# Optimization experiments

Hardware: AMD Instinct MI355X
Metric: run time of the kernel (lower is better)

The kernel has to match this reference:

```python
import jax, jax.numpy as jnp
import numpy as np

B, T, V, E, H, NL = 32, 64, 32000, 300, 512, 2
NF, D = 128, 32  # num midi frames, midi_frame_dim
LSTM_IN = E + D  # 332


def setup_inputs() -> dict:
    key = jax.random.key(0)
    ks = jax.random.split(key, 20)
    s = 0.05
    inp = {
        "input_seq": jax.random.randint(ks[0], (B, T), 0, V),
        "midi_sequence": jax.random.normal(ks[1], (B, NF, D), jnp.float32),
        "emb": jax.random.normal(ks[2], (V, E), jnp.float32) * s,
        "mp_w": jax.random.normal(ks[3], (D, D), jnp.float32) * s,
        "mp_b": jnp.zeros((D,), jnp.float32),
        "wh": jax.random.normal(ks[4], (H, H), jnp.float32) * s,
        "wm": jax.random.normal(ks[5], (H, D), jnp.float32) * s,
        "v": jax.random.normal(ks[6], (1, H), jnp.float32) * s,
        "w_ih0": jax.random.normal(ks[7], (4 * H, LSTM_IN), jnp.float32) * s,
        "w_hh0": jax.random.normal(ks[8], (4 * H, H), jnp.float32) * s,
        "b_ih0": jnp.zeros((4 * H,), jnp.float32),
        "b_hh0": jnp.zeros((4 * H,), jnp.float32),
        "w_ih1": jax.random.normal(ks[9], (4 * H, H), jnp.float32) * s,
        "w_hh1": jax.random.normal(ks[10], (4 * H, H), jnp.float32) * s,
        "b_ih1": jnp.zeros((4 * H,), jnp.float32),
        "b_hh1": jnp.zeros((4 * H,), jnp.float32),
        "fc_w": jax.random.uniform(ks[11], (V, H), jnp.float32, -0.1, 0.1),
        "fc_b": jnp.zeros((V,), jnp.float32),
    }
    return inp


def _lstm_cell(x, hp, cp, wih, whh, bih, bhh):
    # PyTorch gate order: i, f, g, o
    g = x @ wih.T + hp @ whh.T + bih + bhh
    i, f, gg, o = jnp.split(g, 4, axis=-1)
    cn = jax.nn.sigmoid(f) * cp + jax.nn.sigmoid(i) * jnp.tanh(gg)
    hn = jax.nn.sigmoid(o) * jnp.tanh(cn)
    return hn, cn


def reference(input_seq, midi_sequence, emb, mp_w, mp_b, wh, wm, v,
              w_ih0, w_hh0, b_ih0, b_hh0, w_ih1, w_hh1, b_ih1, b_hh1,
              fc_w, fc_b):
    embeddings = emb[input_seq]  # [B,T,E] (dropout = identity in eval)
    midi_proj = jax.nn.relu(jnp.einsum('bfd,ed->bfe', midi_sequence, mp_w) + mp_b)  # [B,NF,D]
    midi_key = jnp.einsum('bfd,hd->bfh', midi_proj, wm)  # precomputed W_m(midi_proj)

    h0 = jnp.zeros((NL, B, H), embeddings.dtype)
    c0 = jnp.zeros((NL, B, H), embeddings.dtype)

    def step(carry, x_t):
        h, c = carry
        h_top = h[-1]  # [B,H]
        energy = jnp.tanh((h_top @ wh.T)[:, None, :] + midi_key)  # [B,NF,H]
        scores = jnp.einsum('bfh,h->bf', energy, v[0])
        attn = jax.nn.softmax(scores, axis=-1)  # [B,NF]
        ctx = jnp.einsum('bf,bfd->bd', attn, midi_proj)  # [B,D]
        x = jnp.concatenate([x_t, ctx], axis=-1)  # [B,E+D]
        h1, c1 = _lstm_cell(x, h[0], c[0], w_ih0, w_hh0, b_ih0, b_hh0)
        h2, c2 = _lstm_cell(h1, h[1], c[1], w_ih1, w_hh1, b_ih1, b_hh1)
        return (jnp.stack([h1, h2]), jnp.stack([c1, c2])), (h2, attn)

    (hF, cF), (outs, attns) = jax.lax.scan(step, (h0, c0), embeddings.transpose(1, 0, 2))
    lstm_out = outs.transpose(1, 0, 2)  # [B,T,H]
    logits = lstm_out @ fc_w.T + fc_b  # [B,T,V]
    return logits, (hF, cF), attns.transpose(1, 0, 2)
```

## Files before the change

### kernel.cpp

```cpp
#include <hip/hip_runtime.h>
#include <hip/hip_bf16.h>

#define Bsz 32
#define Tn  64
#define Vn  32000
#define En  300
#define Hn  512
#define NFn 128
#define Dn  32
#define G4  2048
#define LIN 332
#define NWG 256

#define OFF_MPROJ 0
#define OFF_E0    (OFF_MPROJ + 131072)
#define OFF_PG0B  (OFF_E0 + 4194304)
#define OFF_H1T   (OFF_PG0B + 65536)
#define OFF_H2T0  (OFF_H1T + 16384)
#define OFF_H2T1  (OFF_H2T0 + 16384)
#define OFF_H2BB  (OFF_H2T1 + 16384)
#define OFF_C1T   (OFF_H2BB + 16384)
#define OFF_C2T   (OFF_C1T + 16384)
#define OFF_FLG   (OFF_C2T + 16384)
#define OFF_DONE  (OFF_FLG + 4096)
#define OFF_VC    (OFF_DONE + 256)
#define OFF_MKEY  (OFF_VC + 16)
#define OFF_WHT   (OFF_MKEY + 2097152)
#define OFF_WCTX  (OFF_WHT + 262144)
#define OFF_X     (OFF_WCTX + 65536)
#define OFF_W0    (OFF_X + 655360)
#define OFF_HBF   OFF_X
#define OFF_FCWBF (OFF_X + 524288)

#define O_H1S  0
#define O_H2S  1048576
#define O_QS   2113536
#define O_CTXP 3162112
#define O_DENP 3686400
#define O_ES   3702784

#define OUT_HF  65536000
#define OUT_CF  65568768
#define OUT_ATT 65601536

#define L_HS2   0
#define L_HS1   4096
#define L_GL    8192
#define L_PG0   8480
#define L_C1    8736
#define L_C2    8800
#define L_CTX   8864
#define L_DEN   9128
#define L_QL    9136
#define L_VL    9664
#define L_SP    10192
#define L_ESL   10464
#define L_CP    10480
#define L_W0    11024
#define L_MK    27408
#define L_WH    35856
#define SCAN_LDS_FLOATS 39952
#define SCAN_LDS_BYTES  (SCAN_LDS_FLOATS*4)

typedef __attribute__((ext_vector_type(8))) short short8;
typedef __attribute__((ext_vector_type(4))) float f32x4;
typedef unsigned short u16;

__device__ __forceinline__ float frcp(float x){ return __builtin_amdgcn_rcpf(x); }
__device__ __forceinline__ float ftanh(float x){
  float e = __expf(2.0f*x);
  return 1.0f - 2.0f*frcp(e+1.0f);
}
__device__ __forceinline__ float fsig(float x){
  return frcp(1.0f + __expf(-x));
}
__device__ __forceinline__ u16 f2bf(float f){
  __hip_bfloat16 h = __float2bfloat16(f);
  u16 r; __builtin_memcpy(&r, &h, 2); return r;
}

__device__ __forceinline__ float ldc1(const float* p){
  return __hip_atomic_load(p, __ATOMIC_RELAXED, __HIP_MEMORY_SCOPE_AGENT);
}
__device__ __forceinline__ void stc1(float* p, float v){
  __hip_atomic_store(p, v, __ATOMIC_RELAXED, __HIP_MEMORY_SCOPE_AGENT);
}

__device__ __forceinline__ void flag_store(float* ws, int c, int slot, float v){
  stc1(ws + OFF_FLG + c*256 + slot*4, v);
}
__device__ __forceinline__ void aggregate(float* ws, int c, float tgt, int tid){
  if (tid < 64){
    const float* fl = ws + OFF_FLG + c*256;
    unsigned cc = 0;
    while (true){
      float v = ldc1(fl + tid*4);
      if (__ballot(v >= tgt) == ~0ull) break;
      if (++cc >= (1u<<22)) break;
    }
    if (tid == 0) stc1(ws + OFF_DONE + c*16, tgt);
  }
}
__device__ __forceinline__ void waitD(float* ws, int c, float tgt){
  __syncthreads();
  if (threadIdx.x == 0){
    unsigned cc = 0;
    while (ldc1(ws + OFF_DONE + c*16) < tgt){
      if (++cc >= (1u<<24)) break;
    }
  }
  __syncthreads();
  asm volatile("" ::: "memory");
}

__device__ __forceinline__ float redux32(float (&v)[32], int L){
  #pragma unroll
  for (int i=0;i<5;i++){
    const int m = 1<<i, h = 16>>i;
    const bool up = (L & m);
    #pragma unroll
    for (int u=0; u<h; u++){
      float send = up ? v[u] : v[u+h];
      float keep = up ? v[u+h] : v[u];
      v[u] = keep + __shfl_xor(send, m, 64);
    }
  }
  v[0] += __shfl_xor(v[0], 32, 64);
  return v[0];
}
__device__ __forceinline__ float redux16(float (&v)[16], int L){
  #pragma unroll
  for (int i=0;i<4;i++){
    const int m = 1<<i, h = 8>>i;
    const bool up = (L & m);
    #pragma unroll
    for (int u=0; u<h; u++){
      float send = up ? v[u] : v[u+h];
      float keep = up ? v[u+h] : v[u];
      v[u] = keep + __shfl_xor(send, m, 64);
    }
  }
  v[0] += __shfl_xor(v[0], 16, 64);
  v[0] += __shfl_xor(v[0], 32, 64);
  return v[0];
}

__global__ __launch_bounds__(1024) void p1_midi(
    const float* __restrict__ midi, const float* __restrict__ mp_w,
    const float* __restrict__ mp_b, const float* __restrict__ wm,
    float* __restrict__ ws)
{
  __shared__ float ms[NFn*Dn];
  __shared__ float pj[NFn*33];
  __shared__ float mpw[Dn*33];
  __shared__ float mpb[Dn];
  int b = blockIdx.x, tid = threadIdx.x;
  for (int i=tid;i<NFn*Dn;i+=1024) ms[i] = midi[b*NFn*Dn + i];
  { int e = tid>>5, d = tid&31; mpw[e*33+d] = mp_w[tid]; }
  if (tid < Dn) mpb[tid] = mp_b[tid];
  __syncthreads();
  float* mproj = ws + OFF_MPROJ;
  for (int i=tid;i<NFn*Dn;i+=1024){
    int f = i>>5, e = i&31;
    float a = mpb[e];
    #pragma unroll
    for (int d=0;d<Dn;d++) a += ms[f*32+d]*mpw[e*33+d];
    a = fmaxf(a, 0.0f);
    pj[f*33+e] = a;
    mproj[b*NFn*Dn + i] = a;
  }
  __syncthreads();
  int h = tid & 511, fh = tid >> 9;
  float wreg[32];
  #pragma unroll
  for (int d=0;d<32;d++) wreg[d] = wm[h*32+d];
  float* mkf = ws + OFF_MKEY + b*(NFn*Hn);
  for (int ff=0; ff<64; ff++){
    int f = fh*64 + ff;
    float a = 0.f;
    #pragma unroll
    for (int d=0;d<32;d++) a += pj[f*33+d]*wreg[d];
    mkf[f*512 + h] = a;
  }
}

__global__ __launch_bounds__(256) void p2a_x(
    const int* __restrict__ seq, const float* __restrict__ emb,
    float* __restrict__ ws)
{
  int idx = blockIdx.x*256 + threadIdx.x;
  int bt = idx / 80, c4 = idx - bt*80;
  int b = bt & 31, t = bt >> 5;
  float4 x = {0.f,0.f,0.f,0.f};
  if (c4 < 75){
    int s = seq[b*Tn + t];
    x = *(const float4*)(emb + (long)s*En + c4*4);
  }
  *(float4*)(ws + OFF_X + bt*320 + c4*4) = x;
}

__global__ __launch_bounds__(256) void p2b_w(
    const float* __restrict__ wih0, float* __restrict__ ws)
{
  int idx = blockIdx.x*256 + threadIdx.x;
  int j = idx / 80, c4 = idx - j*80;
  float4 x = {0.f,0.f,0.f,0.f};
  if (c4 < 75) x = *(const float4*)(wih0 + (long)j*LIN + c4*4);
  *(float4*)(ws + OFF_W0 + j*320 + c4*4) = x;
}

__global__ __launch_bounds__(256) void p2c_e0(
    const float* __restrict__ ws_c, const float* __restrict__ bih0,
    const float* __restrict__ bhh0, float* __restrict__ ws)
{
  const float* A  = ws_c + OFF_W0;
  const float* Bm = ws_c + OFF_X;
  __shared__ float Al[32][132];
  __shared__ float Bl[32][132];
  int tid = threadIdx.x;
  int j0t = blockIdx.x*128, bt0 = blockIdx.y*128;
  int tx = tid & 15, ty = tid >> 4;
  float acc[8][8];
  #pragma unroll
  for (int i=0;i<8;i++)
    #pragma unroll
    for (int j=0;j<8;j++) acc[i][j] = 0.f;

  int m = tid >> 1;
  int kq = (tid & 1) * 16;
  for (int kk=0; kk<320; kk+=32){
    __syncthreads();
    {
      const float* As = A  + (long)(j0t+m)*320 + kk + kq;
      const float* Bs = Bm + (long)(bt0+m)*320 + kk + kq;
      float4 a0 = *(const float4*)(As+0), a1 = *(const float4*)(As+4);
      float4 a2 = *(const float4*)(As+8), a3 = *(const float4*)(As+12);
      float4 b0 = *(const float4*)(Bs+0), b1 = *(const float4*)(Bs+4);
      float4 b2 = *(const float4*)(Bs+8), b3 = *(const float4*)(Bs+12);
      Al[kq+0][m]=a0.x; Al[kq+1][m]=a0.y; Al[kq+2][m]=a0.z; Al[kq+3][m]=a0.w;
      Al[kq+4][m]=a1.x; Al[kq+5][m]=a1.y; Al[kq+6][m]=a1.z; Al[kq+7][m]=a1.w;
      Al[kq+8][m]=a2.x; Al[kq+9][m]=a2.y; Al[kq+10][m]=a2.z; Al[kq+11][m]=a2.w;
      Al[kq+12][m]=a3.x; Al[kq+13][m]=a3.y; Al[kq+14][m]=a3.z; Al[kq+15][m]=a3.w;
      Bl[kq+0][m]=b0.x; Bl[kq+1][m]=b0.y; Bl[kq+2][m]=b0.z; Bl[kq+3][m]=b0.w;
      Bl[kq+4][m]=b1.x; Bl[kq+5][m]=b1.y; Bl[kq+6][m]=b1.z; Bl[kq+7][m]=b1.w;
      Bl[kq+8][m]=b2.x; Bl[kq+9][m]=b2.y; Bl[kq+10][m]=b2.z; Bl[kq+11][m]=b2.w;
      Bl[kq+12][m]=b3.x; Bl[kq+13][m]=b3.y; Bl[kq+14][m]=b3.z; Bl[kq+15][m]=b3.w;
    }
    __syncthreads();
    #pragma unroll 4
    for (int k=0;k<32;k++){
      float4 a0 = *(const float4*)&Al[k][ty*8];
      float4 a1 = *(const float4*)&Al[k][ty*8+4];
      float4 b0 = *(const float4*)&Bl[k][tx*8];
      float4 b1 = *(const float4*)&Bl[k][tx*8+4];
      float av[8] = {a0.x,a0.y,a0.z,a0.w,a1.x,a1.y,a1.z,a1.w};
      float bv[8] = {b0.x,b0.y,b0.z,b0.w,b1.x,b1.y,b1.z,b1.w};
      #pragma unroll
      for (int i=0;i<8;i++)
        #pragma unroll
        for (int j=0;j<8;j++) acc[i][j] += av[i]*bv[j];
    }
  }
  float* E0 = ws + OFF_E0;
  #pragma unroll
  for (int i=0;i<8;i++){
    int j = j0t + ty*8 + i;
    float be = bih0[j] + bhh0[j];
    #pragma unroll
    for (int jj=0;jj<8;jj++){
      int c = bt0 + tx*8 + jj;
      int tt = c >> 5, bb = c & 31;
      E0[tt*65536 + (bb>>3)*16384 + j*8 + (bb&7)] = acc[i][jj] + be;
    }
  }
}

__global__ __launch_bounds__(256) void p3_cvt(
    const float* __restrict__ fcw, float* __restrict__ ws)
{
  u16* dst = (u16*)(ws + OFF_FCWBF);
  int base = (blockIdx.x*256 + threadIdx.x)*8;
  float4 x = *(const float4*)(fcw+base);
  float4 y = *(const float4*)(fcw+base+4);
  short8 p;
  p[0]=(short)f2bf(x.x); p[1]=(short)f2bf(x.y); p[2]=(short)f2bf(x.z); p[3]=(short)f2bf(x.w);
  p[4]=(short)f2bf(y.x); p[5]=(short)f2bf(y.y); p[6]=(short)f2bf(y.z); p[7]=(short)f2bf(y.w);
  *(short8*)(dst+base) = p;
}

__global__ __launch_bounds__(256) void p5_wctx(
    const float* __restrict__ wih0, float* __restrict__ ws)
{
  int idx = blockIdx.x*256 + threadIdx.x;
  int j = idx >> 5, d = idx & 31;
  ws[OFF_WCTX + idx] = wih0[(long)j*LIN + En + d];
}

__global__ __launch_bounds__(512) void p6_vc(
    const float* __restrict__ v, float* __restrict__ ws)
{
  __shared__ float s[8];
  int tid = threadIdx.x;
  float a = fabsf(v[tid]);
  #pragma unroll
  for (int m=1;m<64;m<<=1) a += __shfl_xor(a, m, 64);
  if ((tid&63)==0) s[tid>>6] = a;
  __syncthreads();
  if (tid==0){
    float c=0;
    #pragma unroll
    for (int i=0;i<8;i++) c += s[i];
    ws[OFF_VC] = c;
  }
}

__global__ __launch_bounds__(256) void p0_init(float* __restrict__ ws,
                                               float* __restrict__ out){
  int idx = blockIdx.x*256 + threadIdx.x;
  out[O_H2S + idx] = 0.f;
  if (idx < 4352) ws[OFF_FLG + idx] = 0.f;
}

__global__ __launch_bounds__(256, 1)
void scan_all(
    const float* __restrict__ wih1, const float* __restrict__ whh1,
    const float* __restrict__ whh0, const float* __restrict__ bih1,
    const float* __restrict__ bhh1, const float* __restrict__ wh,
    const float* __restrict__ vvec, float* __restrict__ ws,
    float* __restrict__ out)
{
  extern __shared__ float lds[];
  float* hs2  = lds + L_HS2;
  float* hs1  = lds + L_HS1;
  float* gl   = lds + L_GL;
  float* pg0l = lds + L_PG0;
  float* c1l  = lds + L_C1;
  float* c2l  = lds + L_C2;
  float* ctxl = lds + L_CTX;
  float* denl = lds + L_DEN;
  float* ql   = lds + L_QL;
  float* vl   = lds + L_VL;
  float* sp   = lds + L_SP;
  float* esl  = lds + L_ESL;
  float* cp   = lds + L_CP;
  float* w0l  = lds + L_W0;
  float* mkl  = lds + L_MK;
  float* whl  = lds + L_WH;

  const int wg = blockIdx.x, tid = threadIdx.x;
  const int rg = wg >> 2, bg = wg & 3;
  const int b2 = wg >> 3, fs = wg & 7;
  const int bgp = wg >> 6;
  const int wv = tid >> 6, L = tid & 63;
  u16* hbf = (u16*)(ws + OFF_HBF);

  float w_a[8][8], w_b[8][8];
  #pragma unroll
  for (int r=0;r<8;r++){
    int row = wv*512 + rg*8 + r;
    #pragma unroll
    for (int j=0;j<8;j++){
      w_a[r][j] = wih1[(long)row*512 + j*64 + L];
      w_b[r][j] = whh1[(long)row*512 + j*64 + L];
    }
  }
  for (int c=0; c<64; c++){
    int idx = c*256 + tid;
    int lr = idx >> 9, k = idx & 511;
    int grow = (lr>>3)*512 + rg*8 + (lr&7);
    w0l[idx] = whh0[(long)grow*512 + k];
  }
  for (int c=0; c<32; c++){
    int idx = c*256 + tid;
    int f = idx >> 9, r = idx & 511;
    mkl[f*528 + (r>>5)*33 + (r&31)] =
        ws[OFF_MKEY + b2*65536 + (fs*16+f)*512 + r];
  }
  for (int c=0; c<16; c++){
    int idx = c*256 + tid;
    whl[idx] = wh[(long)(rg*8)*512 + idx];
  }

  const int s4 = ((L&1)<<3) | ((L&2)<<1) | ((L&4)>>1) | ((L&8)>>3);
  const int q_sr = s4 >> 3, q_sx = s4 & 7;
  const int s5 = ((L&1)<<4) | ((L&2)<<2) | (L&4) | ((L&8)>>2) | ((L&16)>>4);
  const int r_sr = s5 >> 3, r_sx = s5 & 7;
  float bsum[2]; int glIdx[2], pgIdx[2];
  #pragma unroll
  for (int p=0;p<2;p++){
    int kk = p*4 + r_sr;
    int row = wv*512 + rg*8 + kk;
    bsum[p] = bih1[row] + bhh1[row];
    glIdx[p] = (wv*8 + kk)*9 + r_sx;
    pgIdx[p] = (wv*8 + kk)*8 + r_sx;
  }

  if (tid < 64){ c1l[tid] = 0.f; c2l[tid] = 0.f; }
  {
    int r = tid>>3, bb = tid&7;
    int row = ((r>>3)<<9) + rg*8 + (r&7);
    pg0l[r*8+bb] = ws[OFF_E0 + bg*16384 + row*8 + bb];
  }
  vl[tid + (tid>>5)] = vvec[tid];
  { int t2 = tid + 256; vl[t2 + (t2>>5)] = vvec[t2]; }
  const float Cv = ws[OFF_VC];
  __syncthreads();

  for (int t=0; t<64; t++){
    const float tgt = (float)(t+1);
    if (t > 0) waitD(ws, 0+bg, (float)t);
    {
      const float* h2b = out + O_H2S + t*16384 + bg*4096;
      float4 v0 = *(const float4*)(h2b +    0 + tid*4);
      float4 v1 = *(const float4*)(h2b + 1024 + tid*4);
      float4 v2 = *(const float4*)(h2b + 2048 + tid*4);
      float4 v3 = *(const float4*)(h2b + 3072 + tid*4);
      int kb = tid >> 1, bb0 = (tid&1)*4;
      hs2[(bb0+0)*512 +   0 + kb] = v0.x; hs2[(bb0+1)*512 +   0 + kb] = v0.y;
      hs2[(bb0+2)*512 +   0 + kb] = v0.z; hs2[(bb0+3)*512 +   0 + kb] = v0.w;
      hs2[(bb0+0)*512 + 128 + kb] = v1.x; hs2[(bb0+1)*512 + 128 + kb] = v1.y;
      hs2[(bb0+2)*512 + 128 + kb] = v1.z; hs2[(bb0+3)*512 + 128 + kb] = v1.w;
      hs2[(bb0+0)*512 + 256 + kb] = v2.x; hs2[(bb0+1)*512 + 256 + kb] = v2.y;
      hs2[(bb0+2)*512 + 256 + kb] = v2.z; hs2[(bb0+3)*512 + 256 + kb] = v2.w;
      hs2[(bb0+0)*512 + 384 + kb] = v3.x; hs2[(bb0+1)*512 + 384 + kb] = v3.y;
      hs2[(bb0+2)*512 + 384 + kb] = v3.z; hs2[(bb0+3)*512 + 384 + kb] = v3.w;
    }
    __syncthreads();
    {
      const float* w0p = whl + (wv*2)*512;
      const float* w1p = w0p + 512;
      float vq[16];
      #pragma unroll
      for (int i=0;i<16;i++) vq[i] = 0.f;
      #pragma unroll
      for (int j=0;j<8;j++){
        int k = j*64 + L;
        float wa = w0p[k], wb = w1p[k];
        #pragma unroll
        for (int x=0;x<8;x++){
          float hv = hs2[x*512+k];
          vq[x] += wa*hv; vq[8+x] += wb*hv;
        }
      }
      float qv = redux16(vq, L);
      if (L < 16)
        stc1(out + O_QS + t*16384 + (bg*8+q_sx)*512 + rg*8 + wv*2 + q_sr, qv);
    }
    __syncthreads();
    if (tid == 0) flag_store(ws, 4+bg, wg>>2, tgt);
    if (wg < 4) aggregate(ws, 4+wg, tgt, tid);

    waitD(ws, 4+bgp, tgt);
    ql[tid + (tid>>5)] = out[O_QS + t*16384 + b2*512 + tid];
    { int t2 = tid + 256; ql[t2 + (t2>>5)] = out[O_QS + t*16384 + b2*512 + t2]; }
    __syncthreads();
    {
      int f = tid>>4, hg = tid&15;
      const float* mkr = mkl + f*528 + hg*33;
      const float* qb = ql + hg*33;
      const float* vb = vl + hg*33;
      float s = 0.f;
      #pragma unroll
      for (int c=0; c<32; c+=4){
        float4 m4 = *(const float4*)(mkr+c);
        s += vb[c+0]*ftanh(qb[c+0]+m4.x) + vb[c+1]*ftanh(qb[c+1]+m4.y)
           + vb[c+2]*ftanh(qb[c+2]+m4.z) + vb[c+3]*ftanh(qb[c+3]+m4.w);
      }
      sp[f*17+hg] = s;
    }
    __syncthreads();
    if (tid < 16){
      float s = 0.f;
      #pragma unroll
      for (int g=0; g<16; g++) s += sp[tid*17+g];
      float e = __expf(s - Cv);
      esl[tid] = e;
      stc1(out + O_ES + t*4096 + b2*128 + fs*16 + tid, e);
    }
    __syncthreads();
    if (tid == 0){
      float d = 0.f;
      #pragma unroll
      for (int i=0;i<16;i++) d += esl[i];
      stc1(out + O_DENP + t*256 + b2*8 + fs, d);
    }
    {
      int d2 = tid&31, f0 = tid>>5;
      cp[d2*17+f0]   = esl[f0]  * ws[OFF_MPROJ + b2*4096 + (fs*16+f0)*32   + d2];
      cp[d2*17+f0+8] = esl[f0+8]* ws[OFF_MPROJ + b2*4096 + (fs*16+f0+8)*32 + d2];
    }
    __syncthreads();
    if (tid < 32){
      float s = 0.f;
      #pragma unroll
      for (int ff=0; ff<16; ff++) s += cp[tid*17+ff];
      stc1(out + O_CTXP + t*8192 + b2*256 + fs*32 + tid, s);
    }
    __syncthreads();
    if (tid == 0) flag_store(ws, 8+bgp, wg&63, tgt);
    if ((wg&63) == 0) aggregate(ws, 8+bgp, tgt, tid);

    waitD(ws, 8+bg, tgt);
    if (tid < 8){
      float dsum = 0.f;
      #pragma unroll
      for (int f2=0; f2<8; f2++) dsum += out[O_DENP + t*256 + (bg*8+tid)*8 + f2];
      denl[tid] = frcp(dsum);
    }
    __syncthreads();
    {
      int bb = tid>>5, d = tid&31;
      float s = 0.f;
      #pragma unroll
      for (int f2=0; f2<8; f2++) s += out[O_CTXP + t*8192 + (bg*8+bb)*256 + f2*32 + d];
      ctxl[bb*33+d] = s * denl[bb];
    }
    if (rg == 0){
      #pragma unroll
      for (int i0=0; i0<4; i0++){
        int i = tid + i0*256;
        int bb = i>>7, f = i&127;
        float e = out[O_ES + t*4096 + (bg*8+bb)*128 + f];
        __builtin_nontemporal_store(e * denl[bb],
            out + OUT_ATT + (bg*8+bb)*8192 + t*128 + f);
      }
    }
    __syncthreads();
    {
      int r = tid>>3, bb = tid&7;
      int row = ((r>>3)<<9) + rg*8 + (r&7);
      float g0 = pg0l[r*8+bb];
      const float* wr = ws + OFF_WCTX + row*32;
      #pragma unroll
      for (int d2=0; d2<32; d2+=4){
        float4 w4 = *(const float4*)(wr+d2);
        g0 += w4.x*ctxl[bb*33+d2] + w4.y*ctxl[bb*33+d2+1]
            + w4.z*ctxl[bb*33+d2+2] + w4.w*ctxl[bb*33+d2+3];
      }
      gl[r*9+bb] = g0;
    }
    __syncthreads();
    if (tid < 64){
      int kk = tid>>3, bb = tid&7;
      float gi = gl[(kk)*9+bb],     gf = gl[(8+kk)*9+bb];
      float gg2 = gl[(16+kk)*9+bb], go = gl[(24+kk)*9+bb];
      float cp2 = c1l[tid];
      float cn = fsig(gf)*cp2 + fsig(gi)*ftanh(gg2);
      float hn = fsig(go)*ftanh(cn);
      c1l[tid] = cn;
      stc1(out + O_H1S + t*16384 + bg*4096 + (rg*8+kk)*8 + bb, hn);
      if (t == 63){
        int bgl = bg*8+bb, kgl = rg*8+kk;
        __builtin_nontemporal_store(hn, out + OUT_HF + bgl*512 + kgl);
        __builtin_nontemporal_store(cn, out + OUT_CF + bgl*512 + kgl);
      }
    }
    __syncthreads();
    if (tid == 0) flag_store(ws, 12+bg, wg>>2, tgt);
    if (wg < 4) aggregate(ws, 12+wg, tgt, tid);

    waitD(ws, 12+bg, tgt);
    {
      const float* h1b = out + O_H1S + t*16384 + bg*4096;
      float4 v0 = *(const float4*)(h1b +    0 + tid*4);
      float4 v1 = *(const float4*)(h1b + 1024 + tid*4);
      float4 v2 = *(const float4*)(h1b + 2048 + tid*4);
      float4 v3 = *(const float4*)(h1b + 3072 + tid*4);
      int kb = tid >> 1, bb0 = (tid&1)*4;
      hs1[(bb0+0)*512 +   0 + kb] = v0.x; hs1[(bb0+1)*512 +   0 + kb] = v0.y;
      hs1[(bb0+2)*512 +   0 + kb] = v0.z; hs1[(bb0+3)*512 +   0 + kb] = v0.w;
      hs1[(bb0+0)*512 + 128 + kb] = v1.x; hs1[(bb0+1)*512 + 128 + kb] = v1.y;
      hs1[(bb0+2)*512 + 128 + kb] = v1.z; hs1[(bb0+3)*512 + 128 + kb] = v1.w;
      hs1[(bb0+0)*512 + 256 + kb] = v2.x; hs1[(bb0+1)*512 + 256 + kb] = v2.y;
      hs1[(bb0+2)*512 + 256 + kb] = v2.z; hs1[(bb0+3)*512 + 256 + kb] = v2.w;
      hs1[(bb0+0)*512 + 384 + kb] = v3.x; hs1[(bb0+1)*512 + 384 + kb] = v3.y;
      hs1[(bb0+2)*512 + 384 + kb] = v3.z; hs1[(bb0+3)*512 + 384 + kb] = v3.w;
    }
    __syncthreads();
    #pragma unroll
    for (int p=0; p<2; p++){
      float vals[32];
      #pragma unroll
      for (int i=0;i<32;i++) vals[i] = 0.f;
      #pragma unroll
      for (int j=0;j<8;j++){
        int k = j*64 + L;
        float h1v[8], h2v[8];
        #pragma unroll
        for (int x=0;x<8;x++){ h1v[x] = hs1[x*512+k]; h2v[x] = hs2[x*512+k]; }
        #pragma unroll
        for (int r=0;r<4;r++){
          const float wa = w_a[p*4+r][j], wb = w_b[p*4+r][j];
          #pragma unroll
          for (int x=0;x<8;x++) vals[r*8+x] += wa*h1v[x] + wb*h2v[x];
        }
      }
      float v0 = redux32(vals, L);
      if (L < 32) gl[glIdx[p]] = v0 + bsum[p];
    }
    __syncthreads();
    if (tid < 64){
      int kk = tid>>3, bb = tid&7;
      float gi = gl[(kk)*9+bb],     gf = gl[(8+kk)*9+bb];
      float gg2 = gl[(16+kk)*9+bb], go = gl[(24+kk)*9+bb];
      float cp3 = c2l[tid];
      float cn = fsig(gf)*cp3 + fsig(gi)*ftanh(gg2);
      float hn = fsig(go)*ftanh(cn);
      c2l[tid] = cn;
      int k2 = rg*8+kk, b = bg*8+bb;
      stc1(out + O_H2S + (t+1)*16384 + bg*4096 + k2*8 + bb, hn);
      __builtin_nontemporal_store(f2bf(hn), hbf + (t*32+b)*512 + k2);
      if (t == 63){
        __builtin_nontemporal_store(hn, out + OUT_HF + 16384 + b*512 + k2);
        __builtin_nontemporal_store(cn, out + OUT_CF + 16384 + b*512 + k2);
      }
    }
    __syncthreads();
    if (tid == 0) flag_store(ws, 0+bg, wg>>2, tgt);
    if (wg < 4) aggregate(ws, 0+wg, tgt, tid);

    if (t < 63){
      #pragma unroll
      for (int p=0; p<2; p++){
        float vals[32];
        #pragma unroll
        for (int i=0;i<32;i++) vals[i] = 0.f;
        #pragma unroll
        for (int j=0;j<8;j++){
          int k = j*64 + L;
          float h1v[8];
          #pragma unroll
          for (int x=0;x<8;x++) h1v[x] = hs1[x*512+k];
          #pragma unroll
          for (int r=0;r<4;r++){
            const float wc = w0l[(wv*8 + p*4 + r)*512 + k];
            #pragma unroll
            for (int x=0;x<8;x++) vals[r*8+x] += wc*h1v[x];
          }
        }
        float v0 = redux32(vals, L);
        if (L < 32) pg0l[pgIdx[p]] = v0;
      }
      __syncthreads();
      {
        int r = tid>>3, bb = tid&7;
        int row = ((r>>3)<<9) + rg*8 + (r&7);
        pg0l[r*8+bb] += __builtin_nontemporal_load(
            ws + OFF_E0 + (t+1)*65536 + bg*16384 + row*8 + bb);
      }
    }
  }
}

__global__ __launch_bounds__(256) void fc_gemm(
    const float* __restrict__ ws_f, const float* __restrict__ fcb,
    float* __restrict__ out)
{
  const u16* A  = (const u16*)(ws_f + OFF_FCWBF);
  const u16* Bm = (const u16*)(ws_f + OFF_HBF);
  __shared__ u16 Al[128*40];
  __shared__ u16 Bl[128*40];
  int tid = threadIdx.x;
  int v0 = blockIdx.x*128, bt0 = blockIdx.y*128;
  int lane = tid & 63, wv = tid >> 6;
  int wr = wv >> 1, wc = wv & 1;
  f32x4 acc[4][4];
  #pragma unroll
  for (int i=0;i<4;i++)
    #pragma unroll
    for (int j=0;j<4;j++) acc[i][j] = (f32x4){0.f,0.f,0.f,0.f};

  int ar = wr*64 + (lane&15);
  int br = wc*64 + (lane&15);
  int ks = (lane>>4)*8;

  for (int kk=0; kk<512; kk+=32){
    __syncthreads();
    #pragma unroll
    for (int i=0;i<2;i++){
      int ld = tid + 256*i;
      int row = ld >> 2, cs = (ld & 3)*8;
      *(int4*)(&Al[row*40+cs]) = *(const int4*)(A  + (v0+row)*512 + kk + cs);
      *(int4*)(&Bl[row*40+cs]) = *(const int4*)(Bm + (bt0+row)*512 + kk + cs);
    }
    __syncthreads();
    short8 af[4], bf[4];
    #pragma unroll
    for (int m=0;m<4;m++) af[m] = *(const short8*)(&Al[(ar+m*16)*40 + ks]);
    #pragma unroll
    for (int n=0;n<4;n++) bf[n] = *(const short8*)(&Bl[(br+n*16)*40 + ks]);
    #pragma unroll
    for (int m=0;m<4;m++)
      #pragma unroll
      for (int n=0;n<4;n++)
        acc[m][n] = __builtin_amdgcn_mfma_f32_16x16x32_bf16(af[m], bf[n], acc[m][n], 0,0,0);
  }
  int r4 = (lane>>4)*4;
  #pragma unroll
  for (int m=0;m<4;m++){
    int v = v0 + wr*64 + m*16 + r4;
    float4 bias = *(const float4*)(fcb + v);
    #pragma unroll
    for (int n=0;n<4;n++){
      int bt = bt0 + wc*64 + n*16 + (lane&15);
      int b = bt & 31, t = bt >> 5;
      f32x4 a = acc[m][n];
      float4 res = { a[0]+bias.x, a[1]+bias.y, a[2]+bias.z, a[3]+bias.w };
      *(float4*)(out + b*2048000 + t*32000 + v) = res;
    }
  }
}

extern "C" void kernel_launch(void* const* d_in, const int* in_sizes, int n_in,
                              void* d_out, int out_size, void* d_ws, size_t ws_size,
                              hipStream_t stream)
{
  const int*   seq  = (const int*)d_in[0];
  const float* midi = (const float*)d_in[1];
  const float* emb  = (const float*)d_in[2];
  const float* mpw  = (const float*)d_in[3];
  const float* mpb  = (const float*)d_in[4];
  const float* wh   = (const float*)d_in[5];
  const float* wm   = (const float*)d_in[6];
  const float* vv   = (const float*)d_in[7];
  const float* wih0 = (const float*)d_in[8];
  const float* whh0 = (const float*)d_in[9];
  const float* bih0 = (const float*)d_in[10];
  const float* bhh0 = (const float*)d_in[11];
  const float* wih1 = (const float*)d_in[12];
  const float* whh1 = (const float*)d_in[13];
  const float* bih1 = (const float*)d_in[14];
  const float* bhh1 = (const float*)d_in[15];
  const float* fcw  = (const float*)d_in[16];
  const float* fcb  = (const float*)d_in[17];
  float* out = (float*)d_out;
  float* ws  = (float*)d_ws;

  hipFuncSetAttribute((const void*)scan_all,
                      hipFuncAttributeMaxDynamicSharedMemorySize,
                      SCAN_LDS_BYTES);

  p1_midi<<<32, 1024, 0, stream>>>(midi, mpw, mpb, wm, ws);
  p2a_x  <<<640, 256, 0, stream>>>(seq, emb, ws);
  p2b_w  <<<640, 256, 0, stream>>>(wih0, ws);
  p2c_e0 <<<dim3(16,16), 256, 0, stream>>>(ws, bih0, bhh0, ws);
  p3_cvt <<<8000, 256, 0, stream>>>(fcw, ws);
  p5_wctx<<<256, 256, 0, stream>>>(wih0, ws);
  p6_vc  <<<1, 512, 0, stream>>>(vv, ws);
  p0_init<<<64, 256, 0, stream>>>(ws, out);

  scan_all<<<NWG, 256, SCAN_LDS_BYTES, stream>>>(wih1, whh1, whh0, bih1, bhh1,
                                                 wh, vv, ws, out);

  fc_gemm<<<dim3(250,16), 256, 0, stream>>>(ws, fcb, out);
}
```

Baseline: 5.566 ms.

## Replace two-level aggregator barrier with direct per-group flag polling

Drops the aggregator scheme, where one workgroup gathered 64 flags and then published a DONE word that everyone else polled. Now every workgroup polls all 64 per-group flags directly with a wavefront ballot. The workgroup index mapping is changed so that the 64 workgroups sharing a batch group are contiguous (rg = wg&63, bg = wg>>6), which makes every stage use the same barrier groups. The aim is to remove one serial hop from each of the four inter-workgroup barriers per timestep. In exchange, many more workgroups poll the flag lines concurrently, which adds memory traffic on those lines.

```diff
diff --git a/kernel.cpp b/kernel.cpp
--- a/kernel.cpp
+++ b/kernel.cpp
@@ -89,7 +89,8 @@
 __device__ __forceinline__ void flag_store(float* ws, int c, int slot, float v){
   stc1(ws + OFF_FLG + c*256 + slot*4, v);
 }
-__device__ __forceinline__ void aggregate(float* ws, int c, float tgt, int tid){
+__device__ __forceinline__ void waitA(float* ws, int c, float tgt, int tid){
+  __syncthreads();
   if (tid < 64){
     const float* fl = ws + OFF_FLG + c*256;
     unsigned cc = 0;
@@ -97,16 +98,6 @@
       float v = ldc1(fl + tid*4);
       if (__ballot(v >= tgt) == ~0ull) break;
       if (++cc >= (1u<<22)) break;
-    }
-    if (tid == 0) stc1(ws + OFF_DONE + c*16, tgt);
-  }
-}
-__device__ __forceinline__ void waitD(float* ws, int c, float tgt){
-  __syncthreads();
-  if (threadIdx.x == 0){
-    unsigned cc = 0;
-    while (ldc1(ws + OFF_DONE + c*16) < tgt){
-      if (++cc >= (1u<<24)) break;
     }
   }
   __syncthreads();
@@ -348,11 +339,12 @@
   float* whl  = lds + L_WH;
 
   const int wg = blockIdx.x, tid = threadIdx.x;
-  const int rg = wg >> 2, bg = wg & 3;
+  const int rg = wg & 63, bg = wg >> 6;
   const int b2 = wg >> 3, fs = wg & 7;
-  const int bgp = wg >> 6;
   const int wv = tid >> 6, L = tid & 63;
   u16* hbf = (u16*)(ws + OFF_HBF);
+
+  const int C_H2 = 0*4+bg, C_Q = 1*4+bg, C_CTX = 2*4+bg, C_H1 = 3*4+bg;
 
   float w_a[8][8], w_b[8][8];
   #pragma unroll
@@ -408,7 +400,7 @@
 
   for (int t=0; t<64; t++){
     const float tgt = (float)(t+1);
-    if (t > 0) waitD(ws, 0+bg, (float)t);
+    if (t > 0) waitA(ws, C_H2, (float)t, tid);
     {
       const float* h2b = out + O_H2S + t*16384 + bg*4096;
       float4 v0 = *(const float4*)(h2b +    0 + tid*4);
@@ -447,10 +439,9 @@
         stc1(out + O_QS + t*16384 + (bg*8+q_sx)*512 + rg*8 + wv*2 + q_sr, qv);
     }
     __syncthreads();
-    if (tid == 0) flag_store(ws, 4+bg, wg>>2, tgt);
-    if (wg < 4) aggregate(ws, 4+wg, tgt, tid);
-
-    waitD(ws, 4+bgp, tgt);
+    if (tid == 0) flag_store(ws, C_Q, rg, tgt);
+
+    waitA(ws, C_Q, tgt, tid);
     ql[tid + (tid>>5)] = out[O_QS + t*16384 + b2*512 + tid];
     { int t2 = tid + 256; ql[t2 + (t2>>5)] = out[O_QS + t*16384 + b2*512 + t2]; }
     __syncthreads();
@@ -497,10 +488,9 @@
       stc1(out + O_CTXP + t*8192 + b2*256 + fs*32 + tid, s);
     }
     __syncthreads();
-    if (tid == 0) flag_store(ws, 8+bgp, wg&63, tgt);
-    if ((wg&63) == 0) aggregate(ws, 8+bgp, tgt, tid);
-
-    waitD(ws, 8+bg, tgt);
+    if (tid == 0) flag_store(ws, C_CTX, rg, tgt);
+
+    waitA(ws, C_CTX, tgt, tid);
     if (tid < 8){
       float dsum = 0.f;
       #pragma unroll
@@ -556,10 +546,9 @@
       }
     }
     __syncthreads();
-    if (tid == 0) flag_store(ws, 12+bg, wg>>2, tgt);
-    if (wg < 4) aggregate(ws, 12+wg, tgt, tid);
-
-    waitD(ws, 12+bg, tgt);
+    if (tid == 0) flag_store(ws, C_H1, rg, tgt);
+
+    waitA(ws, C_H1, tgt, tid);
     {
       const float* h1b = out + O_H1S + t*16384 + bg*4096;
       float4 v0 = *(const float4*)(h1b +    0 + tid*4);
@@ -616,8 +605,7 @@
       }
     }
     __syncthreads();
-    if (tid == 0) flag_store(ws, 0+bg, wg>>2, tgt);
-    if (wg < 4) aggregate(ws, 0+wg, tgt, tid);
+    if (tid == 0) flag_store(ws, C_H2, rg, tgt);
 
     if (t < 63){
       #pragma unroll
```

Result: no change. 5.542 ms (-0.4%).
